# Performance work log

Measured on AMD Instinct MI355X. Metric: run time of the kernel, lower is better.

Reference implementation:

```python
import jax, jax.numpy as jnp
import numpy as np

B, H, S, D = 2, 16, 2048, 128

def setup_inputs() -> dict:
    key = jax.random.key(0)
    kq, kk, kv = jax.random.split(key, 3)
    q = jax.random.normal(kq, (B, H, S, D), dtype=jnp.float32)
    k = jax.random.normal(kk, (B, H, S, D), dtype=jnp.float32)
    v = jax.random.normal(kv, (B, H, S, D), dtype=jnp.float32)
    # causal mask, broadcastable over batch and heads; 0 -> masked out
    mask = jnp.tril(jnp.ones((S, S), dtype=jnp.int32))[None, None, :, :]
    return {"q": q, "k": k, "v": v, "mask": mask}

def reference(q, k, v, mask):
    # scores: [B,H,S,S] -- note: module applies NO 1/sqrt(d) scaling
    attn = jnp.einsum('bhqd,bhkd->bhqk', q, k)
    neg_inf = jnp.finfo(attn.dtype).min
    attn = jnp.where(mask == 0, neg_inf, attn)
    attn = jax.nn.softmax(attn, axis=-1)
    out = jnp.einsum('bhqk,bhkd->bhqd', attn, v)
    return out
```

## Files before the change

kernel.cpp:

```cpp
#include <hip/hip_runtime.h>


#define SQ 2048
#define DH 128
#define BM 64
#define BN 64
#define NELEM 8388608

typedef _Float16 f16x8 __attribute__((ext_vector_type(8)));
typedef float f32x4 __attribute__((ext_vector_type(4)));
typedef unsigned short u16x8 __attribute__((ext_vector_type(8)));
typedef unsigned int u32x4 __attribute__((ext_vector_type(4)));

__device__ __forceinline__ unsigned short f2h(float f) {
  return __builtin_bit_cast(unsigned short, (_Float16)f);
}

__global__ __launch_bounds__(256) void prep(const float* __restrict__ k,
                                            const float* __restrict__ v,
                                            unsigned short* __restrict__ ko,
                                            unsigned short* __restrict__ vt) {
  const int tid = threadIdx.x;
  const int bx = blockIdx.x;
  if (bx < 1024) {
    __shared__ unsigned short lv[64 * 132];
    const int bh = bx >> 5;
    const int s0 = (bx & 31) * 64;
    const float* vs = v + ((size_t)bh * SQ + s0) * DH;
    #pragma unroll
    for (int it = 0; it < 8; ++it) {
      int fi = it * 256 + tid;
      int sL = fi >> 5;
      int dL = (fi & 31) * 4;
      float4 val = *(const float4*)(vs + (size_t)sL * DH + dL);
      ushort4 o;
      o.x = f2h(val.x); o.y = f2h(val.y); o.z = f2h(val.z); o.w = f2h(val.w);
      *(ushort4*)(lv + sL * 132 + dL) = o;
    }
    __syncthreads();
    #pragma unroll
    for (int it = 0; it < 4; ++it) {
      int ci = it * 256 + tid;
      int dL = ci >> 3;
      int sg = ci & 7;
      u16x8 o;
      #pragma unroll
      for (int j = 0; j < 8; ++j) o[j] = lv[(sg * 8 + j) * 132 + dL];
      *(u16x8*)(vt + ((size_t)bh * DH + dL) * SQ + s0 + sg * 8) = o;
    }
  } else {
    const int NT = NELEM / 4;
    for (int i = (bx - 1024) * 256 + tid; i < NT; i += 2048 * 256) {
      float4 val = ((const float4*)k)[i];
      ushort4 o;
      o.x = f2h(val.x); o.y = f2h(val.y); o.z = f2h(val.z); o.w = f2h(val.w);
      ((ushort4*)ko)[i] = o;
    }
  }
}

__global__ __launch_bounds__(256, 4) void fattn(const float* __restrict__ Qf,
                                                const unsigned short* __restrict__ Kh,
                                                const unsigned short* __restrict__ Vth,
                                                float* __restrict__ Out) {
  __shared__ char smem[40960];
  const int tid  = threadIdx.x;
  const int wave = tid >> 6;
  const int lane = tid & 63;
  const int quad = lane >> 4;
  const int c    = lane & 15;

  const int t     = (int)blockIdx.x;
  const int xcd   = t & 7;
  const int idx   = t >> 3;
  const int cu    = idx & 31;
  const int round = idx >> 5;
  const int bh    = xcd * 4 + round;
  int qb;
  {
    int b0 = (cu + 8 * (round >> 1)) & 31;
    qb = (round & 1) ? (31 - b0) : b0;
  }
  const int rowbase = qb * BM;

  char* sK = smem;
  char* sV = smem + 16384;
  char* sP = smem + 32768 + wave * 2048;

  const float* Qg = Qf + ((size_t)bh * SQ + rowbase) * DH;
  #pragma unroll
  for (int it = 0; it < 8; ++it) {
    int gi  = it * 256 + tid;
    int row = gi >> 5;
    int sub = gi & 31;
    float4 qv = *(const float4*)(Qg + (size_t)row * DH + sub * 4);
    ushort4 h;
    h.x = f2h(qv.x); h.y = f2h(qv.y); h.z = f2h(qv.z); h.w = f2h(qv.w);
    int gr = (sub >> 1) ^ (row & 7);
    *(ushort4*)(smem + row * 256 + gr * 16 + (sub & 1) * 8) = h;
  }
  __syncthreads();
  f16x8 qf[4];
  {
    int rl = wave * 16 + c;
    #pragma unroll
    for (int ch = 0; ch < 4; ++ch) {
      int gr = (ch * 4 + quad) ^ (c & 7);
      qf[ch] = *(const f16x8*)(smem + rl * 256 + gr * 16);
    }
  }

  const unsigned short* Kbase = Kh + (size_t)bh * SQ * DH;
  const unsigned short* Vbase = Vth + (size_t)bh * DH * SQ;
  const unsigned short* Ksrc = Kbase + (size_t)(tid >> 4) * DH
                             + ((tid & 15) ^ ((tid >> 4) & 7)) * 8;
  const unsigned short* Vsrc = Vbase + (size_t)(tid >> 3) * SQ
                             + ((tid & 7) ^ ((tid >> 3) & 7)) * 8;

  u32x4 kreg[4], vreg[4];
  #pragma unroll
  for (int it = 0; it < 4; ++it)
    kreg[it] = *(const u32x4*)(Ksrc + it * (16 * DH));
  #pragma unroll
  for (int it = 0; it < 4; ++it)
    vreg[it] = *(const u32x4*)(Vsrc + it * (32 * SQ));
  __syncthreads();

  #pragma unroll
  for (int it = 0; it < 4; ++it)
    *(u32x4*)(sK + it * 4096 + tid * 16) = kreg[it];
  #pragma unroll
  for (int it = 0; it < 4; ++it)
    *(u32x4*)(sV + it * 4096 + tid * 16) = vreg[it];
  __syncthreads();

  f32x4 acc[8];
  #pragma unroll
  for (int dt = 0; dt < 8; ++dt) acc[dt] = (f32x4){0.f, 0.f, 0.f, 0.f};
  float mo = -1e30f, lrow = 0.f;

  const int nkt = qb + 1;
  for (int kt = 0; kt < nkt; ++kt) {
    if (kt + 1 < nkt) {
      const unsigned short* Kn = Ksrc + (size_t)(kt + 1) * (BN * DH);
      const unsigned short* Vn = Vsrc + (size_t)(kt + 1) * BN;
      #pragma unroll
      for (int it = 0; it < 4; ++it)
        kreg[it] = *(const u32x4*)(Kn + it * (16 * DH));
      #pragma unroll
      for (int it = 0; it < 4; ++it)
        vreg[it] = *(const u32x4*)(Vn + it * (32 * SQ));
    }
    __builtin_amdgcn_sched_barrier(0);

    const bool diag  = (kt == qb);
    const int ntmax  = diag ? wave : 3;
    const int chmax  = diag ? (wave >> 1) : 1;

    f32x4 sc[4];
    #pragma unroll
    for (int nt = 0; nt < 4; ++nt) sc[nt] = (f32x4){0.f, 0.f, 0.f, 0.f};
    __builtin_amdgcn_s_setprio(1);
    #pragma unroll
    for (int nt = 0; nt < 4; ++nt) {
      if (nt <= ntmax) {
        int keyl = nt * 16 + c;
        #pragma unroll
        for (int ch = 0; ch < 4; ++ch) {
          int gr = (ch * 4 + quad) ^ (c & 7);
          f16x8 kf = *(const f16x8*)(sK + keyl * 256 + gr * 16);
          sc[nt] = __builtin_amdgcn_mfma_f32_16x16x32_f16(kf, qf[ch], sc[nt], 0, 0, 0);
        }
      }
    }
    __builtin_amdgcn_s_setprio(0);

    if (diag) {
      int rl = wave * 16 + c;
      #pragma unroll
      for (int nt = 0; nt < 4; ++nt)
        #pragma unroll
        for (int r = 0; r < 4; ++r)
          if (nt * 16 + quad * 4 + r > rl) sc[nt][r] = -1e30f;
    }

    float cm = -1e30f;
    #pragma unroll
    for (int nt = 0; nt < 4; ++nt)
      #pragma unroll
      for (int r = 0; r < 4; ++r) cm = fmaxf(cm, sc[nt][r]);
    cm = fmaxf(cm, __shfl_xor(cm, 16));
    cm = fmaxf(cm, __shfl_xor(cm, 32));
    float mn = fmaxf(mo, cm);
    float al = __expf(mo - mn);
    float rs = 0.f;
    ushort4 pk[4];
    #pragma unroll
    for (int nt = 0; nt < 4; ++nt) {
      #pragma unroll
      for (int r = 0; r < 4; ++r) {
        float p = __expf(sc[nt][r] - mn);
        rs += p;
        ((unsigned short*)&pk[nt])[r] = f2h(p);
      }
    }
    rs += __shfl_xor(rs, 16);
    rs += __shfl_xor(rs, 32);
    lrow = lrow * al + rs;
    mo = mn;
    #pragma unroll
    for (int dt = 0; dt < 8; ++dt) acc[dt] *= al;

    #pragma unroll
    for (int nt = 0; nt < 4; ++nt) {
      int g8 = nt * 2 + (quad >> 1);
      *(ushort4*)(sP + c * 128 + ((g8 ^ (c & 7)) * 16) + (quad & 1) * 8) = pk[nt];
    }

    __builtin_amdgcn_s_setprio(1);
    #pragma unroll
    for (int ch = 0; ch < 2; ++ch) {
      if (ch <= chmax) {
        f16x8 pf = *(const f16x8*)(sP + c * 128 + (((ch * 4 + quad) ^ (c & 7)) * 16));
        #pragma unroll
        for (int dt = 0; dt < 8; ++dt) {
          int d  = dt * 16 + c;
          int gr = (ch * 4 + quad) ^ (c & 7);
          f16x8 vf = *(const f16x8*)(sV + d * 128 + gr * 16);
          acc[dt] = __builtin_amdgcn_mfma_f32_16x16x32_f16(vf, pf, acc[dt], 0, 0, 0);
        }
      }
    }
    __builtin_amdgcn_s_setprio(0);

    if (kt + 1 < nkt) {
      __syncthreads();
      #pragma unroll
      for (int it = 0; it < 4; ++it)
        *(u32x4*)(sK + it * 4096 + tid * 16) = kreg[it];
      #pragma unroll
      for (int it = 0; it < 4; ++it)
        *(u32x4*)(sV + it * 4096 + tid * 16) = vreg[it];
      __syncthreads();
    }
  }

  const float inv = 1.0f / lrow;
  const int rowg = rowbase + wave * 16 + c;
  float* op = Out + ((size_t)bh * SQ + rowg) * DH;
  #pragma unroll
  for (int dt = 0; dt < 8; ++dt) {
    float4 o;
    o.x = acc[dt][0] * inv;
    o.y = acc[dt][1] * inv;
    o.z = acc[dt][2] * inv;
    o.w = acc[dt][3] * inv;
    *(float4*)(op + dt * 16 + quad * 4) = o;
  }
}

extern "C" void kernel_launch(void* const* d_in, const int* in_sizes, int n_in,
                              void* d_out, int out_size, void* d_ws, size_t ws_size,
                              hipStream_t stream) {
  const float* q = (const float*)d_in[0];
  const float* k = (const float*)d_in[1];
  const float* v = (const float*)d_in[2];
  float* out = (float*)d_out;

  unsigned short* kws = (unsigned short*)d_ws;
  unsigned short* vws = kws + NELEM;

  prep<<<3072, 256, 0, stream>>>(k, v, kws, vws);
  fattn<<<1024, 256, 0, stream>>>(q, kws, vws, out);
}
```

Before: 207.9 us.

## Use exp2 with prescaled Q, lazy rescale, and split K/V smem refill barriers

```diff
diff --git a/kernel.cpp b/kernel.cpp
--- a/kernel.cpp
+++ b/kernel.cpp
@@ -8,9 +8,11 @@
 #define NELEM 8388608
 
 typedef _Float16 f16x8 __attribute__((ext_vector_type(8)));
+typedef _Float16 f16x2 __attribute__((ext_vector_type(2)));
 typedef float f32x4 __attribute__((ext_vector_type(4)));
 typedef unsigned short u16x8 __attribute__((ext_vector_type(8)));
 typedef unsigned int u32x4 __attribute__((ext_vector_type(4)));
+typedef unsigned int u32x2 __attribute__((ext_vector_type(2)));
 
 __device__ __forceinline__ unsigned short f2h(float f) {
   return __builtin_bit_cast(unsigned short, (_Float16)f);
@@ -87,6 +89,7 @@
   char* sV = smem + 16384;
   char* sP = smem + 32768 + wave * 2048;
 
+  const float L2E = 1.44269504088896f;
   const float* Qg = Qf + ((size_t)bh * SQ + rowbase) * DH;
   #pragma unroll
   for (int it = 0; it < 8; ++it) {
@@ -95,7 +98,8 @@
     int sub = gi & 31;
     float4 qv = *(const float4*)(Qg + (size_t)row * DH + sub * 4);
     ushort4 h;
-    h.x = f2h(qv.x); h.y = f2h(qv.y); h.z = f2h(qv.z); h.w = f2h(qv.w);
+    h.x = f2h(qv.x * L2E); h.y = f2h(qv.y * L2E);
+    h.z = f2h(qv.z * L2E); h.w = f2h(qv.w * L2E);
     int gr = (sub >> 1) ^ (row & 7);
     *(ushort4*)(smem + row * 256 + gr * 16 + (sub & 1) * 8) = h;
   }
@@ -141,7 +145,8 @@
 
   const int nkt = qb + 1;
   for (int kt = 0; kt < nkt; ++kt) {
-    if (kt + 1 < nkt) {
+    const bool hn = (kt + 1 < nkt);
+    if (hn) {
       const unsigned short* Kn = Ksrc + (size_t)(kt + 1) * (BN * DH);
       const unsigned short* Vn = Vsrc + (size_t)(kt + 1) * BN;
       #pragma unroll
@@ -175,6 +180,13 @@
     }
     __builtin_amdgcn_s_setprio(0);
 
+    __syncthreads();
+    if (hn) {
+      #pragma unroll
+      for (int it = 0; it < 4; ++it)
+        *(u32x4*)(sK + it * 4096 + tid * 16) = kreg[it];
+    }
+
     if (diag) {
       int rl = wave * 16 + c;
       #pragma unroll
@@ -184,37 +196,49 @@
           if (nt * 16 + quad * 4 + r > rl) sc[nt][r] = -1e30f;
     }
 
-    float cm = -1e30f;
-    #pragma unroll
-    for (int nt = 0; nt < 4; ++nt)
-      #pragma unroll
-      for (int r = 0; r < 4; ++r) cm = fmaxf(cm, sc[nt][r]);
+    f32x4 ta, tb;
+    #pragma unroll
+    for (int r = 0; r < 4; ++r) {
+      ta[r] = fmaxf(sc[0][r], sc[1][r]);
+      tb[r] = fmaxf(sc[2][r], sc[3][r]);
+    }
+    float cm = fmaxf(fmaxf(fmaxf(ta[0], tb[0]), fmaxf(ta[1], tb[1])),
+                     fmaxf(fmaxf(ta[2], tb[2]), fmaxf(ta[3], tb[3])));
     cm = fmaxf(cm, __shfl_xor(cm, 16));
     cm = fmaxf(cm, __shfl_xor(cm, 32));
-    float mn = fmaxf(mo, cm);
-    float al = __expf(mo - mn);
-    float rs = 0.f;
-    ushort4 pk[4];
+    const bool keep = __all(cm <= mo + 8.0f) != 0;
+    const float mn = keep ? mo : fmaxf(mo, cm);
+
+    float ps[4];
+    u32x2 pkd[4];
     #pragma unroll
     for (int nt = 0; nt < 4; ++nt) {
-      #pragma unroll
-      for (int r = 0; r < 4; ++r) {
-        float p = __expf(sc[nt][r] - mn);
-        rs += p;
-        ((unsigned short*)&pk[nt])[r] = f2h(p);
-      }
-    }
+      float p0 = __builtin_amdgcn_exp2f(sc[nt][0] - mn);
+      float p1 = __builtin_amdgcn_exp2f(sc[nt][1] - mn);
+      float p2 = __builtin_amdgcn_exp2f(sc[nt][2] - mn);
+      float p3 = __builtin_amdgcn_exp2f(sc[nt][3] - mn);
+      ps[nt] = (p0 + p1) + (p2 + p3);
+      pkd[nt][0] = __builtin_bit_cast(unsigned int, __builtin_amdgcn_cvt_pkrtz(p0, p1));
+      pkd[nt][1] = __builtin_bit_cast(unsigned int, __builtin_amdgcn_cvt_pkrtz(p2, p3));
+    }
+    float rs = (ps[0] + ps[1]) + (ps[2] + ps[3]);
     rs += __shfl_xor(rs, 16);
     rs += __shfl_xor(rs, 32);
-    lrow = lrow * al + rs;
-    mo = mn;
-    #pragma unroll
-    for (int dt = 0; dt < 8; ++dt) acc[dt] *= al;
 
     #pragma unroll
     for (int nt = 0; nt < 4; ++nt) {
       int g8 = nt * 2 + (quad >> 1);
-      *(ushort4*)(sP + c * 128 + ((g8 ^ (c & 7)) * 16) + (quad & 1) * 8) = pk[nt];
+      *(u32x2*)(sP + c * 128 + ((g8 ^ (c & 7)) * 16) + (quad & 1) * 8) = pkd[nt];
+    }
+
+    if (keep) {
+      lrow += rs;
+    } else {
+      const float al = __builtin_amdgcn_exp2f(mo - mn);
+      lrow = lrow * al + rs;
+      mo = mn;
+      #pragma unroll
+      for (int dt = 0; dt < 8; ++dt) acc[dt] *= al;
     }
 
     __builtin_amdgcn_s_setprio(1);
@@ -233,15 +257,11 @@
     }
     __builtin_amdgcn_s_setprio(0);
 
-    if (kt + 1 < nkt) {
+    if (hn) {
       __syncthreads();
       #pragma unroll
       for (int it = 0; it < 4; ++it)
-        *(u32x4*)(sK + it * 4096 + tid * 16) = kreg[it];
-      #pragma unroll
-      for (int it = 0; it < 4; ++it)
         *(u32x4*)(sV + it * 4096 + tid * 16) = vreg[it];
-      __syncthreads();
     }
   }
 
```

After: 205.0 us. About the same (-1.4%).
